# Performance work log

Hardware: AMD Instinct MI355X
Metric: run time of the kernel (lower is better)

Reference implementation:

```python
import jax, jax.numpy as jnp
import numpy as np

FP8_MAX = 448.0   # e4m3 max finite value
BLOCK = 128


def _cast_e4m3(v):
    """Fake-cast to fp8 e4m3: round to nearest representable value (3 mantissa bits,
    min normal exponent -6, subnormal step 2^-9), saturate at +-448."""
    a = jnp.minimum(jnp.abs(v), FP8_MAX)
    e = jnp.floor(jnp.log2(jnp.maximum(a, jnp.float32(2.0) ** -9)))
    e = jnp.maximum(e, -6.0)                 # subnormal range
    step = jnp.exp2(e - 3.0)                 # 3 mantissa bits
    q = jnp.round(a / step) * step
    q = jnp.minimum(q, FP8_MAX)
    return jnp.sign(v) * q


def fake_quant_blockwise(x, br, bc):
    """Per-(br x bc)-tile scale = amax/448, cast to e4m3, dequantize."""
    R, C = x.shape
    xt = x.reshape(R // br, br, C // bc, bc)
    amax = jnp.max(jnp.abs(xt), axis=(1, 3), keepdims=True)
    scale = jnp.maximum(amax, 1e-12) / FP8_MAX
    q = _cast_e4m3(xt / scale) * scale
    return q.reshape(R, C)


def setup_inputs() -> dict:
    key = jax.random.key(0)
    k1, k2 = jax.random.split(key)
    x = jax.random.normal(k1, (8192, 4096), dtype=jnp.float32)
    weight = jax.random.normal(k2, (4096, 4096), dtype=jnp.float32) * 0.02
    bias = jnp.zeros((4096,), dtype=jnp.float32)
    return {"x": x, "weight": weight, "bias": bias}


def reference(x, weight, bias):
    # activations: per-row 1x128 blocks (is_left); weight: 128x128 square tiles (is_sqtile)
    x_fq = fake_quant_blockwise(x, 1, BLOCK)
    w_fq = fake_quant_blockwise(weight, BLOCK, BLOCK)
    return jnp.einsum('ti,oi->to', x_fq, w_fq) + bias
```

## Files before the change

### kernel.cpp

```cpp
#include <hip/hip_runtime.h>

#define M_DIM 8192
#define N_DIM 4096
#define K_DIM 4096

typedef __bf16 bf16x8 __attribute__((ext_vector_type(8)));
typedef float f32x4 __attribute__((ext_vector_type(4)));

__device__ __forceinline__ unsigned short f2bf(float f) {
    unsigned u = __float_as_uint(f);
    u += 0x7FFFu + ((u >> 16) & 1u);
    return (unsigned short)(u >> 16);
}

__device__ __forceinline__ float cast_e4m3(float v) {
    float a = fminf(fabsf(v), 448.0f);
    float am = fmaxf(a, 0x1p-9f);
    int e = (int)((__float_as_uint(am) >> 23) & 0xFFu) - 127;
    e = (e < -6) ? -6 : e;
    float step = __uint_as_float((unsigned)(e - 3 + 127) << 23);
    float q = rintf(a / step) * step;
    q = fminf(q, 448.0f);
    return (v < 0.0f) ? -q : q;
}

__global__ __launch_bounds__(256) void quant_x(const float* __restrict__ X,
                                               unsigned short* __restrict__ Xq) {
    const int g = threadIdx.x >> 5;
    const int l = threadIdx.x & 31;
    const long rb = (long)blockIdx.x * 8 + g;
    const int row = (int)(rb >> 5);
    const int kb = (int)(rb & 31);
    const size_t base = (size_t)row * K_DIM + kb * 128 + l * 4;
    const float4 v = *(const float4*)&X[base];
    float amax = fmaxf(fmaxf(fabsf(v.x), fabsf(v.y)), fmaxf(fabsf(v.z), fabsf(v.w)));
    #pragma unroll
    for (int m = 16; m >= 1; m >>= 1)
        amax = fmaxf(amax, __shfl_xor(amax, m));
    const float scale = fmaxf(amax, 1e-12f) / 448.0f;
    ushort4 o;
    o.x = f2bf(cast_e4m3(v.x / scale) * scale);
    o.y = f2bf(cast_e4m3(v.y / scale) * scale);
    o.z = f2bf(cast_e4m3(v.z / scale) * scale);
    o.w = f2bf(cast_e4m3(v.w / scale) * scale);
    *(ushort4*)&Xq[base] = o;
}

__global__ __launch_bounds__(256) void quant_w(const float* __restrict__ W,
                                               unsigned short* __restrict__ Wq) {
    const int tile = blockIdx.x;
    const int tr = tile >> 5;
    const int tc = tile & 31;
    const int t = threadIdx.x;
    const int c4 = (t & 31) * 4;
    const float* base = W + (size_t)(tr * 128) * K_DIM + tc * 128;

    float4 v[16];
    float amax = 0.0f;
    #pragma unroll
    for (int p = 0; p < 16; ++p) {
        const int r = p * 8 + (t >> 5);
        v[p] = *(const float4*)&base[(size_t)r * K_DIM + c4];
        amax = fmaxf(amax, fmaxf(fmaxf(fabsf(v[p].x), fabsf(v[p].y)),
                                 fmaxf(fabsf(v[p].z), fabsf(v[p].w))));
    }
    #pragma unroll
    for (int m = 32; m >= 1; m >>= 1)
        amax = fmaxf(amax, __shfl_xor(amax, m));
    __shared__ float red[4];
    if ((t & 63) == 0) red[t >> 6] = amax;
    __syncthreads();
    const float am4 = fmaxf(fmaxf(red[0], red[1]), fmaxf(red[2], red[3]));
    const float scale = fmaxf(am4, 1e-12f) / 448.0f;

    unsigned short* out = Wq + (size_t)(tr * 128) * K_DIM + tc * 128;
    #pragma unroll
    for (int p = 0; p < 16; ++p) {
        const int r = p * 8 + (t >> 5);
        ushort4 o;
        o.x = f2bf(cast_e4m3(v[p].x / scale) * scale);
        o.y = f2bf(cast_e4m3(v[p].y / scale) * scale);
        o.z = f2bf(cast_e4m3(v[p].z / scale) * scale);
        o.w = f2bf(cast_e4m3(v[p].w / scale) * scale);
        *(ushort4*)&out[(size_t)r * K_DIM + c4] = o;
    }
}

#define GLOAD16(g, l)                                                          \
    __builtin_amdgcn_global_load_lds(                                          \
        (const __attribute__((address_space(1))) void*)(g),                    \
        (__attribute__((address_space(3))) void*)(l), 16, 0, 0)


#define BARRIER() __builtin_amdgcn_s_barrier()
#define LGKM0() asm volatile("s_waitcnt lgkmcnt(0)" ::: "memory")
#define LGKM8() asm volatile("s_waitcnt lgkmcnt(8)" ::: "memory")
#define VM6()   asm volatile("s_waitcnt vmcnt(6)" ::: "memory")
#define VM0()   asm volatile("s_waitcnt vmcnt(0)" ::: "memory")

#define STAGE(G, grow0, kt, ebase, ht) do {                                    \
    const int _kt = (kt) > 63 ? 63 : (kt);                                     \
    const unsigned short* _s0 = (G) +                                          \
        (size_t)((grow0) + (ht) * 128 + w * 8 + sr) * K_DIM + _kt * 64 + src_col; \
    const unsigned short* _s1 = _s0 + (size_t)64 * K_DIM;                      \
    char* _lb = (char*)lds + (ebase) * 2 + ((ht) * 128 + w * 8) * 128;         \
    GLOAD16(_s0, _lb);                                                         \
    GLOAD16(_s1, _lb + 8192);                                                  \
} while (0)

#define LDA(mh, ebase) do {                                                    \
    _Pragma("unroll") for (int _m = 0; _m < 4; ++_m) {                         \
        const int _row = wm * 128 + (mh) * 64 + _m * 16 + lr;                  \
        a[_m][0] = *(const bf16x8*)&lds[(ebase) + _row * 64 + ((0  + hk) ^ rsw)]; \
        a[_m][1] = *(const bf16x8*)&lds[(ebase) + _row * 64 + ((32 + hk) ^ rsw)]; \
    }                                                                          \
} while (0)

#define LDB(nh, dst, ebase) do {                                               \
    _Pragma("unroll") for (int _n = 0; _n < 2; ++_n) {                         \
        const int _row = wn * 64 + (nh) * 32 + _n * 16 + lr;                   \
        dst[_n][0] = *(const bf16x8*)&lds[(ebase) + _row * 64 + ((0  + hk) ^ rsw)]; \
        dst[_n][1] = *(const bf16x8*)&lds[(ebase) + _row * 64 + ((32 + hk) ^ rsw)]; \
    }                                                                          \
} while (0)

#define MMA(mh, nh, bb) do {                                                   \
    _Pragma("unroll") for (int _m = 0; _m < 4; ++_m)                           \
    _Pragma("unroll") for (int _n = 0; _n < 2; ++_n)                           \
    _Pragma("unroll") for (int _k = 0; _k < 2; ++_k)                           \
        acc[(mh) * 4 + _m][(nh) * 2 + _n] =                                    \
            __builtin_amdgcn_mfma_f32_16x16x32_bf16(                           \
                a[_m][_k], bb[_n][_k], acc[(mh) * 4 + _m][(nh) * 2 + _n], 0, 0, 0); \
} while (0)

#define PRIO1() __builtin_amdgcn_s_setprio(1)
#define PRIO0() __builtin_amdgcn_s_setprio(0)

__global__ __launch_bounds__(512, 2) void gemm256(const unsigned short* __restrict__ A,
                                                  const unsigned short* __restrict__ B,
                                                  const float* __restrict__ bias,
                                                  float* __restrict__ C) {
    __shared__ __align__(16) unsigned short lds[65536];

    const int t = threadIdx.x;
    const int lane = t & 63;
    const int w = t >> 6;
    const int wm = w >> 2, wn = w & 3;

    int bid = blockIdx.x;
    bid = (bid & 7) * 64 + (bid >> 3);
    const int bm = bid >> 4, bn = bid & 15;
    const size_t brow = (size_t)bm * 256, bcol = (size_t)bn * 256;

    const int sr = lane >> 3;
    const int src_col = (((lane & 7) ^ ((lane >> 3) & 7)) << 3);
    const int lr = lane & 15;
    const int hk = (lane >> 4) * 8;
    const int rsw = (lane & 7) << 3;

    f32x4 acc[8][4] = {};
    bf16x8 a[4][2], b0[2][2], b1[2][2];

    STAGE(A, brow, 0, 0, 0);     STAGE(A, brow, 0, 0, 1);
    STAGE(B, bcol, 0, 32768, 0); STAGE(B, bcol, 0, 32768, 1);
    STAGE(B, bcol, 1, 49152, 0); STAGE(B, bcol, 1, 49152, 1);
    STAGE(A, brow, 1, 16384, 0);
    VM6(); BARRIER();

    for (int u = 0; u < 64; u += 2) {
        LDA(0, 0); LDB(0, b0, 32768); LDB(1, b1, 32768);
        STAGE(A, brow, u + 1, 16384, 1);
        LGKM8();
        BARRIER(); LGKM0();
        PRIO1(); MMA(0, 0, b0); PRIO0();
        BARRIER();
        STAGE(B, bcol, u + 2, 32768, 0);
        BARRIER();
        PRIO1(); MMA(0, 1, b1); PRIO0();
        BARRIER();
        LDA(1, 0);
        STAGE(B, bcol, u + 2, 32768, 1);
        BARRIER(); LGKM0();
        PRIO1(); MMA(1, 1, b1); PRIO0();
        BARRIER();
        STAGE(A, brow, u + 2, 0, 0);
        BARRIER();
        PRIO1(); MMA(1, 0, b0); PRIO0();
        VM6();
        BARRIER();
        LDA(0, 16384); LDB(0, b0, 49152); LDB(1, b1, 49152);
        STAGE(A, brow, u + 2, 0, 1);
        LGKM8();
        BARRIER(); LGKM0();
        PRIO1(); MMA(0, 0, b0); PRIO0();
        BARRIER();
        STAGE(B, bcol, u + 3, 49152, 0);
        BARRIER();
        PRIO1(); MMA(0, 1, b1); PRIO0();
        BARRIER();
        LDA(1, 16384);
        STAGE(B, bcol, u + 3, 49152, 1);
        BARRIER(); LGKM0();
        PRIO1(); MMA(1, 1, b1); PRIO0();
        BARRIER();
        STAGE(A, brow, u + 3, 16384, 0);
        BARRIER();
        PRIO1(); MMA(1, 0, b0); PRIO0();
        VM6();
        BARRIER();
    }

    VM0();

    #pragma unroll
    for (int i = 0; i < 8; ++i) {
        const size_t row_base = brow + wm * 128 + i * 16 + (lane >> 4) * 4;
        #pragma unroll
        for (int j = 0; j < 4; ++j) {
            const size_t col = bcol + wn * 64 + j * 16 + lr;
            const float bv = bias[col];
            #pragma unroll
            for (int jj = 0; jj < 4; ++jj)
                C[(row_base + jj) * (size_t)N_DIM + col] = acc[i][j][jj] + bv;
        }
    }
}

extern "C" void kernel_launch(void* const* d_in, const int* in_sizes, int n_in,
                              void* d_out, int out_size, void* d_ws, size_t ws_size,
                              hipStream_t stream) {
    const float* x = (const float*)d_in[0];
    const float* w = (const float*)d_in[1];
    const float* bias = (const float*)d_in[2];
    float* out = (float*)d_out;

    unsigned short* xq = (unsigned short*)d_ws;
    unsigned short* wq = xq + (size_t)M_DIM * K_DIM;

    quant_x<<<(M_DIM * (K_DIM / 128)) / 8, 256, 0, stream>>>(x, xq);
    quant_w<<<(N_DIM / 128) * (K_DIM / 128), 256, 0, stream>>>(w, wq);
    gemm256<<<(M_DIM / 256) * (N_DIM / 256), 512, 0, stream>>>(xq, wq, bias, out);
}
```

Measured before the change: 293.8 us.

## Double-buffer LDS fragment registers to overlap reads with MFMA in GEMM loop

Rewrites the GEMM main loop schedule to use separate register fragments (a0/a1, b0e/b0o) so LDS reads for the next sub-tile are issued before the current MFMA block. It also cuts the barriers per half-iteration from eight to four and replaces full lgkmcnt(0) waits with partial counts. The point is to hide LDS latency and barrier stalls behind matrix instructions. The cost is more live registers, and the finer wait counts may hide ordering hazards between async global-to-LDS loads and reads.

```diff
diff --git a/kernel.cpp b/kernel.cpp
--- a/kernel.cpp
+++ b/kernel.cpp
@@ -93,10 +93,11 @@
 
 
 #define BARRIER() __builtin_amdgcn_s_barrier()
-#define LGKM0() asm volatile("s_waitcnt lgkmcnt(0)" ::: "memory")
-#define LGKM8() asm volatile("s_waitcnt lgkmcnt(8)" ::: "memory")
-#define VM6()   asm volatile("s_waitcnt vmcnt(6)" ::: "memory")
-#define VM0()   asm volatile("s_waitcnt vmcnt(0)" ::: "memory")
+#define FENCE()  asm volatile("" ::: "memory")
+#define LGKM(n)  asm volatile("s_waitcnt lgkmcnt(" #n ")" ::: "memory")
+#define VMC(n)   asm volatile("s_waitcnt vmcnt(" #n ")" ::: "memory")
+#define PRIO1()  __builtin_amdgcn_s_setprio(1)
+#define PRIO0()  __builtin_amdgcn_s_setprio(0)
 
 #define STAGE(G, grow0, kt, ebase, ht) do {                                    \
     const int _kt = (kt) > 63 ? 63 : (kt);                                     \
@@ -108,15 +109,15 @@
     GLOAD16(_s1, _lb + 8192);                                                  \
 } while (0)
 
-#define LDA(mh, ebase) do {                                                    \
+#define LDA(dst, mh, ebase) do {                                               \
     _Pragma("unroll") for (int _m = 0; _m < 4; ++_m) {                         \
         const int _row = wm * 128 + (mh) * 64 + _m * 16 + lr;                  \
-        a[_m][0] = *(const bf16x8*)&lds[(ebase) + _row * 64 + ((0  + hk) ^ rsw)]; \
-        a[_m][1] = *(const bf16x8*)&lds[(ebase) + _row * 64 + ((32 + hk) ^ rsw)]; \
+        dst[_m][0] = *(const bf16x8*)&lds[(ebase) + _row * 64 + ((0  + hk) ^ rsw)]; \
+        dst[_m][1] = *(const bf16x8*)&lds[(ebase) + _row * 64 + ((32 + hk) ^ rsw)]; \
     }                                                                          \
 } while (0)
 
-#define LDB(nh, dst, ebase) do {                                               \
+#define LDB(dst, nh, ebase) do {                                               \
     _Pragma("unroll") for (int _n = 0; _n < 2; ++_n) {                         \
         const int _row = wn * 64 + (nh) * 32 + _n * 16 + lr;                   \
         dst[_n][0] = *(const bf16x8*)&lds[(ebase) + _row * 64 + ((0  + hk) ^ rsw)]; \
@@ -124,17 +125,19 @@
     }                                                                          \
 } while (0)
 
-#define MMA(mh, nh, bb) do {                                                   \
+#define MMA(aA, mh, nh, bB) do {                                               \
     _Pragma("unroll") for (int _m = 0; _m < 4; ++_m)                           \
     _Pragma("unroll") for (int _n = 0; _n < 2; ++_n)                           \
     _Pragma("unroll") for (int _k = 0; _k < 2; ++_k)                           \
         acc[(mh) * 4 + _m][(nh) * 2 + _n] =                                    \
             __builtin_amdgcn_mfma_f32_16x16x32_bf16(                           \
-                a[_m][_k], bb[_n][_k], acc[(mh) * 4 + _m][(nh) * 2 + _n], 0, 0, 0); \
-} while (0)
-
-#define PRIO1() __builtin_amdgcn_s_setprio(1)
-#define PRIO0() __builtin_amdgcn_s_setprio(0)
+                aA[_m][_k], bB[_n][_k], acc[(mh) * 4 + _m][(nh) * 2 + _n], 0, 0, 0); \
+} while (0)
+
+#define AE 0
+#define AO 16384
+#define BE 32768
+#define BO 49152
 
 __global__ __launch_bounds__(512, 2) void gemm256(const unsigned short* __restrict__ A,
                                                   const unsigned short* __restrict__ B,
@@ -159,58 +162,57 @@
     const int rsw = (lane & 7) << 3;
 
     f32x4 acc[8][4] = {};
-    bf16x8 a[4][2], b0[2][2], b1[2][2];
-
-    STAGE(A, brow, 0, 0, 0);     STAGE(A, brow, 0, 0, 1);
-    STAGE(B, bcol, 0, 32768, 0); STAGE(B, bcol, 0, 32768, 1);
-    STAGE(B, bcol, 1, 49152, 0); STAGE(B, bcol, 1, 49152, 1);
-    STAGE(A, brow, 1, 16384, 0);
-    VM6(); BARRIER();
+    bf16x8 a0[4][2], a1[4][2], b0e[2][2], b0o[2][2], b1[2][2];
+
+    STAGE(A, brow, 0, AE, 0); STAGE(A, brow, 0, AE, 1);
+    STAGE(B, bcol, 0, BE, 0); STAGE(B, bcol, 0, BE, 1);
+    STAGE(B, bcol, 1, BO, 0); STAGE(B, bcol, 1, BO, 1);
+    VMC(4); BARRIER(); FENCE();
+    LDA(a0, 0, AE); LDB(b0e, 0, BE);
+    FENCE();
 
     for (int u = 0; u < 64; u += 2) {
-        LDA(0, 0); LDB(0, b0, 32768); LDB(1, b1, 32768);
-        STAGE(A, brow, u + 1, 16384, 1);
-        LGKM8();
-        BARRIER(); LGKM0();
-        PRIO1(); MMA(0, 0, b0); PRIO0();
-        BARRIER();
-        STAGE(B, bcol, u + 2, 32768, 0);
-        BARRIER();
-        PRIO1(); MMA(0, 1, b1); PRIO0();
-        BARRIER();
-        LDA(1, 0);
-        STAGE(B, bcol, u + 2, 32768, 1);
-        BARRIER(); LGKM0();
-        PRIO1(); MMA(1, 1, b1); PRIO0();
-        BARRIER();
-        STAGE(A, brow, u + 2, 0, 0);
-        BARRIER();
-        PRIO1(); MMA(1, 0, b0); PRIO0();
-        VM6();
-        BARRIER();
-        LDA(0, 16384); LDB(0, b0, 49152); LDB(1, b1, 49152);
-        STAGE(A, brow, u + 2, 0, 1);
-        LGKM8();
-        BARRIER(); LGKM0();
-        PRIO1(); MMA(0, 0, b0); PRIO0();
-        BARRIER();
-        STAGE(B, bcol, u + 3, 49152, 0);
-        BARRIER();
-        PRIO1(); MMA(0, 1, b1); PRIO0();
-        BARRIER();
-        LDA(1, 16384);
-        STAGE(B, bcol, u + 3, 49152, 1);
-        BARRIER(); LGKM0();
-        PRIO1(); MMA(1, 1, b1); PRIO0();
-        BARRIER();
-        STAGE(A, brow, u + 3, 16384, 0);
-        BARRIER();
-        PRIO1(); MMA(1, 0, b0); PRIO0();
-        VM6();
-        BARRIER();
-    }
-
-    VM0();
+        LDB(b1, 1, BE);
+        STAGE(A, brow, u + 1, AO, 0); STAGE(A, brow, u + 1, AO, 1);
+        LGKM(4);
+        PRIO1(); MMA(a0, 0, 0, b0e); PRIO0();
+        BARRIER(); FENCE();
+        LDA(a1, 1, AE);
+        LGKM(8);
+        PRIO1(); MMA(a0, 0, 1, b1); PRIO0();
+        BARRIER(); FENCE();
+        STAGE(B, bcol, u + 2, BE, 0);
+        LGKM(0);
+        PRIO1(); MMA(a1, 1, 1, b1); PRIO0();
+        VMC(2);
+        BARRIER(); FENCE();
+        LDA(a0, 0, AO); LDB(b0o, 0, BO);
+        STAGE(B, bcol, u + 2, BE, 1);
+        PRIO1(); MMA(a1, 1, 0, b0e); PRIO0();
+        BARRIER(); FENCE();
+
+        LDB(b1, 1, BO);
+        STAGE(A, brow, u + 2, AE, 0); STAGE(A, brow, u + 2, AE, 1);
+        LGKM(4);
+        PRIO1(); MMA(a0, 0, 0, b0o); PRIO0();
+        BARRIER(); FENCE();
+        LDA(a1, 1, AO);
+        LGKM(8);
+        PRIO1(); MMA(a0, 0, 1, b1); PRIO0();
+        BARRIER(); FENCE();
+        STAGE(B, bcol, u + 3, BO, 0);
+        LGKM(0);
+        PRIO1(); MMA(a1, 1, 1, b1); PRIO0();
+        VMC(2);
+        BARRIER(); FENCE();
+        LDA(a0, 0, AE); LDB(b0e, 0, BE);
+        STAGE(B, bcol, u + 3, BO, 1);
+        PRIO1(); MMA(a1, 1, 0, b0o); PRIO0();
+        BARRIER(); FENCE();
+    }
+
+    LGKM(0); VMC(0);
+    BARRIER();
 
     #pragma unroll
     for (int i = 0; i < 8; ++i) {
```

Measured after the change: 324.9 us. +10.6%, slower.

## Halve GEMM K-tile to 32 and shrink LDS to 64KB

Applied to the files above, without the earlier changes.

Changes the main bf16 GEMM's K step from 64 to 32, so each stage holds half the data and LDS drops from 128KB to 64KB. The load swizzle, wait counts and stage schedule are reworked to match, and the loop runs twice as many iterations. The smaller LDS footprint may ease occupancy or scheduling with two blocks per CU. In exchange there are twice as many barriers and loop iterations per unit of MMA work, and less latency hiding per stage.

```diff
diff --git a/kernel.cpp b/kernel.cpp
--- a/kernel.cpp
+++ b/kernel.cpp
@@ -94,53 +94,50 @@
 
 #define BARRIER() __builtin_amdgcn_s_barrier()
 #define LGKM0() asm volatile("s_waitcnt lgkmcnt(0)" ::: "memory")
-#define LGKM8() asm volatile("s_waitcnt lgkmcnt(8)" ::: "memory")
-#define VM6()   asm volatile("s_waitcnt vmcnt(6)" ::: "memory")
+#define VM2()   asm volatile("s_waitcnt vmcnt(2)" ::: "memory")
 #define VM0()   asm volatile("s_waitcnt vmcnt(0)" ::: "memory")
+#define PRIO1() __builtin_amdgcn_s_setprio(1)
+#define PRIO0() __builtin_amdgcn_s_setprio(0)
 
 #define STAGE(G, grow0, kt, ebase, ht) do {                                    \
-    const int _kt = (kt) > 63 ? 63 : (kt);                                     \
-    const unsigned short* _s0 = (G) +                                          \
-        (size_t)((grow0) + (ht) * 128 + w * 8 + sr) * K_DIM + _kt * 64 + src_col; \
-    const unsigned short* _s1 = _s0 + (size_t)64 * K_DIM;                      \
-    char* _lb = (char*)lds + (ebase) * 2 + ((ht) * 128 + w * 8) * 128;         \
-    GLOAD16(_s0, _lb);                                                         \
-    GLOAD16(_s1, _lb + 8192);                                                  \
+    const int _kt = (kt) > 127 ? 127 : (kt);                                   \
+    const unsigned short* _s = (G) +                                           \
+        (size_t)((grow0) + (ht) * 128 + (t >> 2)) * K_DIM + _kt * 32 + src_e;  \
+    GLOAD16(_s, (char*)lds + (ebase) * 2 + (ht) * 8192 + w * 1024);            \
 } while (0)
 
 #define LDA(mh, ebase) do {                                                    \
     _Pragma("unroll") for (int _m = 0; _m < 4; ++_m) {                         \
         const int _row = wm * 128 + (mh) * 64 + _m * 16 + lr;                  \
-        a[_m][0] = *(const bf16x8*)&lds[(ebase) + _row * 64 + ((0  + hk) ^ rsw)]; \
-        a[_m][1] = *(const bf16x8*)&lds[(ebase) + _row * 64 + ((32 + hk) ^ rsw)]; \
+        a[_m] = *(const bf16x8*)&lds[(ebase) + _row * 32 + rde];               \
     }                                                                          \
 } while (0)
 
 #define LDB(nh, dst, ebase) do {                                               \
     _Pragma("unroll") for (int _n = 0; _n < 2; ++_n) {                         \
         const int _row = wn * 64 + (nh) * 32 + _n * 16 + lr;                   \
-        dst[_n][0] = *(const bf16x8*)&lds[(ebase) + _row * 64 + ((0  + hk) ^ rsw)]; \
-        dst[_n][1] = *(const bf16x8*)&lds[(ebase) + _row * 64 + ((32 + hk) ^ rsw)]; \
+        dst[_n] = *(const bf16x8*)&lds[(ebase) + _row * 32 + rde];             \
     }                                                                          \
 } while (0)
 
 #define MMA(mh, nh, bb) do {                                                   \
     _Pragma("unroll") for (int _m = 0; _m < 4; ++_m)                           \
     _Pragma("unroll") for (int _n = 0; _n < 2; ++_n)                           \
-    _Pragma("unroll") for (int _k = 0; _k < 2; ++_k)                           \
         acc[(mh) * 4 + _m][(nh) * 2 + _n] =                                    \
             __builtin_amdgcn_mfma_f32_16x16x32_bf16(                           \
-                a[_m][_k], bb[_n][_k], acc[(mh) * 4 + _m][(nh) * 2 + _n], 0, 0, 0); \
-} while (0)
-
-#define PRIO1() __builtin_amdgcn_s_setprio(1)
-#define PRIO0() __builtin_amdgcn_s_setprio(0)
+                a[_m], bb[_n], acc[(mh) * 4 + _m][(nh) * 2 + _n], 0, 0, 0);    \
+} while (0)
+
+#define A0E 0
+#define A1E 8192
+#define B0E 16384
+#define B1E 24576
 
 __global__ __launch_bounds__(512, 2) void gemm256(const unsigned short* __restrict__ A,
                                                   const unsigned short* __restrict__ B,
                                                   const float* __restrict__ bias,
                                                   float* __restrict__ C) {
-    __shared__ __align__(16) unsigned short lds[65536];
+    __shared__ __align__(16) unsigned short lds[32768];
 
     const int t = threadIdx.x;
     const int lane = t & 63;
@@ -152,61 +149,58 @@
     const int bm = bid >> 4, bn = bid & 15;
     const size_t brow = (size_t)bm * 256, bcol = (size_t)bn * 256;
 
-    const int sr = lane >> 3;
-    const int src_col = (((lane & 7) ^ ((lane >> 3) & 7)) << 3);
+    const int src_e = ((lane & 3) ^ ((t >> 3) & 3)) * 8;
     const int lr = lane & 15;
-    const int hk = (lane >> 4) * 8;
-    const int rsw = (lane & 7) << 3;
+    const int rde = (((lane >> 4) ^ (lane >> 1)) & 3) << 3;
 
     f32x4 acc[8][4] = {};
-    bf16x8 a[4][2], b0[2][2], b1[2][2];
-
-    STAGE(A, brow, 0, 0, 0);     STAGE(A, brow, 0, 0, 1);
-    STAGE(B, bcol, 0, 32768, 0); STAGE(B, bcol, 0, 32768, 1);
-    STAGE(B, bcol, 1, 49152, 0); STAGE(B, bcol, 1, 49152, 1);
-    STAGE(A, brow, 1, 16384, 0);
-    VM6(); BARRIER();
-
-    for (int u = 0; u < 64; u += 2) {
-        LDA(0, 0); LDB(0, b0, 32768); LDB(1, b1, 32768);
-        STAGE(A, brow, u + 1, 16384, 1);
-        LGKM8();
+    bf16x8 a[4], b0[2], b1[2];
+
+    STAGE(A, brow, 0, A0E, 0); STAGE(A, brow, 0, A0E, 1);
+    STAGE(B, bcol, 0, B0E, 0); STAGE(B, bcol, 0, B0E, 1);
+    STAGE(B, bcol, 1, B1E, 0); STAGE(B, bcol, 1, B1E, 1);
+    VM2(); BARRIER();
+
+    for (int u = 0; u < 128; u += 2) {
+        LDA(0, A0E); LDB(0, b0, B0E);
+        STAGE(A, brow, u + 1, A1E, 0);
         BARRIER(); LGKM0();
         PRIO1(); MMA(0, 0, b0); PRIO0();
         BARRIER();
-        STAGE(B, bcol, u + 2, 32768, 0);
-        BARRIER();
+        LDB(1, b1, B0E);
+        STAGE(A, brow, u + 1, A1E, 1);
+        BARRIER(); LGKM0();
         PRIO1(); MMA(0, 1, b1); PRIO0();
         BARRIER();
-        LDA(1, 0);
-        STAGE(B, bcol, u + 2, 32768, 1);
+        LDA(1, A0E);
+        STAGE(B, bcol, u + 2, B0E, 0);
         BARRIER(); LGKM0();
         PRIO1(); MMA(1, 1, b1); PRIO0();
         BARRIER();
-        STAGE(A, brow, u + 2, 0, 0);
+        STAGE(B, bcol, u + 2, B0E, 1);
         BARRIER();
         PRIO1(); MMA(1, 0, b0); PRIO0();
-        VM6();
-        BARRIER();
-        LDA(0, 16384); LDB(0, b0, 49152); LDB(1, b1, 49152);
-        STAGE(A, brow, u + 2, 0, 1);
-        LGKM8();
+        VM2();
+        BARRIER();
+        LDA(0, A1E); LDB(0, b0, B1E);
+        STAGE(A, brow, u + 2, A0E, 0);
         BARRIER(); LGKM0();
         PRIO1(); MMA(0, 0, b0); PRIO0();
         BARRIER();
-        STAGE(B, bcol, u + 3, 49152, 0);
-        BARRIER();
+        LDB(1, b1, B1E);
+        STAGE(A, brow, u + 2, A0E, 1);
+        BARRIER(); LGKM0();
         PRIO1(); MMA(0, 1, b1); PRIO0();
         BARRIER();
-        LDA(1, 16384);
-        STAGE(B, bcol, u + 3, 49152, 1);
+        LDA(1, A1E);
+        STAGE(B, bcol, u + 3, B1E, 0);
         BARRIER(); LGKM0();
         PRIO1(); MMA(1, 1, b1); PRIO0();
         BARRIER();
-        STAGE(A, brow, u + 3, 16384, 0);
+        STAGE(B, bcol, u + 3, B1E, 1);
         BARRIER();
         PRIO1(); MMA(1, 0, b0); PRIO0();
-        VM6();
+        VM2();
         BARRIER();
     }
 
```

Result: slower. 304.3 us (+3.6%).

## Switch GEMM inner loop to 32x32x16 bf16 MFMA with rescheduled staging

Applied to the files above, without the earlier changes.

Replaces the 16x16x32 MFMA tiles with 32x32x16 MFMA instructions, changing the per-wave fragment layout, LDS read pattern, and epilogue store mapping. The prefetch schedule is also reordered so LDS reads are interleaved between MFMA groups, with a different vmcnt wait depth. The larger MFMA shape is meant to cut the number of LDS fragment reads and instructions per FLOP. In exchange it changes the staging order and the output store pattern, which may affect latency hiding and write coalescing.

```diff
diff --git a/kernel.cpp b/kernel.cpp
--- a/kernel.cpp
+++ b/kernel.cpp
@@ -5,7 +5,7 @@
 #define K_DIM 4096
 
 typedef __bf16 bf16x8 __attribute__((ext_vector_type(8)));
-typedef float f32x4 __attribute__((ext_vector_type(4)));
+typedef float f32x16 __attribute__((ext_vector_type(16)));
 
 __device__ __forceinline__ unsigned short f2bf(float f) {
     unsigned u = __float_as_uint(f);
@@ -95,8 +95,10 @@
 #define BARRIER() __builtin_amdgcn_s_barrier()
 #define LGKM0() asm volatile("s_waitcnt lgkmcnt(0)" ::: "memory")
 #define LGKM8() asm volatile("s_waitcnt lgkmcnt(8)" ::: "memory")
-#define VM6()   asm volatile("s_waitcnt vmcnt(6)" ::: "memory")
+#define VM4()   asm volatile("s_waitcnt vmcnt(4)" ::: "memory")
 #define VM0()   asm volatile("s_waitcnt vmcnt(0)" ::: "memory")
+#define PRIO1() __builtin_amdgcn_s_setprio(1)
+#define PRIO0() __builtin_amdgcn_s_setprio(0)
 
 #define STAGE(G, grow0, kt, ebase, ht) do {                                    \
     const int _kt = (kt) > 63 ? 63 : (kt);                                     \
@@ -108,33 +110,28 @@
     GLOAD16(_s1, _lb + 8192);                                                  \
 } while (0)
 
-#define LDA(mh, ebase) do {                                                    \
-    _Pragma("unroll") for (int _m = 0; _m < 4; ++_m) {                         \
-        const int _row = wm * 128 + (mh) * 64 + _m * 16 + lr;                  \
-        a[_m][0] = *(const bf16x8*)&lds[(ebase) + _row * 64 + ((0  + hk) ^ rsw)]; \
-        a[_m][1] = *(const bf16x8*)&lds[(ebase) + _row * 64 + ((32 + hk) ^ rsw)]; \
+#define LDA32(mh) do {                                                         \
+    _Pragma("unroll") for (int _f = 0; _f < 2; ++_f) {                         \
+        const int _row = wm * 128 + (mh) * 64 + _f * 32 + l31;                 \
+        _Pragma("unroll") for (int _k = 0; _k < 4; ++_k)                       \
+            a[_f][_k] = *(const bf16x8*)&lds[abase + _row * 64 +               \
+                                             ((_k * 16 + hk32) ^ rsw)];        \
     }                                                                          \
 } while (0)
 
-#define LDB(nh, dst, ebase) do {                                               \
-    _Pragma("unroll") for (int _n = 0; _n < 2; ++_n) {                         \
-        const int _row = wn * 64 + (nh) * 32 + _n * 16 + lr;                   \
-        dst[_n][0] = *(const bf16x8*)&lds[(ebase) + _row * 64 + ((0  + hk) ^ rsw)]; \
-        dst[_n][1] = *(const bf16x8*)&lds[(ebase) + _row * 64 + ((32 + hk) ^ rsw)]; \
-    }                                                                          \
-} while (0)
-
-#define MMA(mh, nh, bb) do {                                                   \
-    _Pragma("unroll") for (int _m = 0; _m < 4; ++_m)                           \
-    _Pragma("unroll") for (int _n = 0; _n < 2; ++_n)                           \
-    _Pragma("unroll") for (int _k = 0; _k < 2; ++_k)                           \
-        acc[(mh) * 4 + _m][(nh) * 2 + _n] =                                    \
-            __builtin_amdgcn_mfma_f32_16x16x32_bf16(                           \
-                a[_m][_k], bb[_n][_k], acc[(mh) * 4 + _m][(nh) * 2 + _n], 0, 0, 0); \
-} while (0)
-
-#define PRIO1() __builtin_amdgcn_s_setprio(1)
-#define PRIO0() __builtin_amdgcn_s_setprio(0)
+#define LDB32(nh, dst) do {                                                    \
+    const int _row = wn * 64 + (nh) * 32 + l31;                                \
+    _Pragma("unroll") for (int _k = 0; _k < 4; ++_k)                           \
+        dst[_k] = *(const bf16x8*)&lds[bbase + _row * 64 +                     \
+                                       ((_k * 16 + hk32) ^ rsw)];              \
+} while (0)
+
+#define MMA32(mh, nh, bb) do {                                                 \
+    _Pragma("unroll") for (int _k = 0; _k < 4; ++_k)                           \
+    _Pragma("unroll") for (int _f = 0; _f < 2; ++_f)                           \
+        acc[(mh) * 2 + _f][nh] = __builtin_amdgcn_mfma_f32_32x32x16_bf16(      \
+            a[_f][_k], bb[_k], acc[(mh) * 2 + _f][nh], 0, 0, 0);               \
+} while (0)
 
 __global__ __launch_bounds__(512, 2) void gemm256(const unsigned short* __restrict__ A,
                                                   const unsigned short* __restrict__ B,
@@ -154,74 +151,81 @@
 
     const int sr = lane >> 3;
     const int src_col = (((lane & 7) ^ ((lane >> 3) & 7)) << 3);
-    const int lr = lane & 15;
-    const int hk = (lane >> 4) * 8;
+    const int l31 = lane & 31;
+    const int hk32 = (lane >> 5) * 8;
     const int rsw = (lane & 7) << 3;
 
-    f32x4 acc[8][4] = {};
-    bf16x8 a[4][2], b0[2][2], b1[2][2];
+    f32x16 acc[4][2] = {};
+    bf16x8 a[2][4], b0[4], b1[4];
+    int abase, bbase;
 
     STAGE(A, brow, 0, 0, 0);     STAGE(A, brow, 0, 0, 1);
     STAGE(B, bcol, 0, 32768, 0); STAGE(B, bcol, 0, 32768, 1);
     STAGE(B, bcol, 1, 49152, 0); STAGE(B, bcol, 1, 49152, 1);
-    STAGE(A, brow, 1, 16384, 0);
-    VM6(); BARRIER();
+    VM4(); BARRIER();
 
     for (int u = 0; u < 64; u += 2) {
-        LDA(0, 0); LDB(0, b0, 32768); LDB(1, b1, 32768);
+        abase = 0; bbase = 32768;
+        LDA32(0); LDB32(0, b0);
+        STAGE(A, brow, u + 1, 16384, 0);
+        LGKM8();
+        BARRIER(); LGKM0();
+        PRIO1(); MMA32(0, 0, b0); PRIO0();
+        BARRIER();
+        LDB32(1, b1);
         STAGE(A, brow, u + 1, 16384, 1);
+        BARRIER(); LGKM0();
+        PRIO1(); MMA32(0, 1, b1); PRIO0();
+        BARRIER();
+        LDA32(1);
+        STAGE(B, bcol, u + 2, 32768, 0);
+        BARRIER(); LGKM0();
+        PRIO1(); MMA32(1, 1, b1); PRIO0();
+        BARRIER();
+        STAGE(B, bcol, u + 2, 32768, 1);
+        BARRIER();
+        PRIO1(); MMA32(1, 0, b0); PRIO0();
+        VM4();
+        BARRIER();
+        abase = 16384; bbase = 49152;
+        LDA32(0); LDB32(0, b0);
+        STAGE(A, brow, u + 2, 0, 0);
         LGKM8();
         BARRIER(); LGKM0();
-        PRIO1(); MMA(0, 0, b0); PRIO0();
-        BARRIER();
-        STAGE(B, bcol, u + 2, 32768, 0);
-        BARRIER();
-        PRIO1(); MMA(0, 1, b1); PRIO0();
-        BARRIER();
-        LDA(1, 0);
-        STAGE(B, bcol, u + 2, 32768, 1);
-        BARRIER(); LGKM0();
-        PRIO1(); MMA(1, 1, b1); PRIO0();
-        BARRIER();
-        STAGE(A, brow, u + 2, 0, 0);
-        BARRIER();
-        PRIO1(); MMA(1, 0, b0); PRIO0();
-        VM6();
-        BARRIER();
-        LDA(0, 16384); LDB(0, b0, 49152); LDB(1, b1, 49152);
+        PRIO1(); MMA32(0, 0, b0); PRIO0();
+        BARRIER();
+        LDB32(1, b1);
         STAGE(A, brow, u + 2, 0, 1);
-        LGKM8();
-        BARRIER(); LGKM0();
-        PRIO1(); MMA(0, 0, b0); PRIO0();
-        BARRIER();
+        BARRIER(); LGKM0();
+        PRIO1(); MMA32(0, 1, b1); PRIO0();
+        BARRIER();
+        LDA32(1);
         STAGE(B, bcol, u + 3, 49152, 0);
-        BARRIER();
-        PRIO1(); MMA(0, 1, b1); PRIO0();
-        BARRIER();
-        LDA(1, 16384);
+        BARRIER(); LGKM0();
+        PRIO1(); MMA32(1, 1, b1); PRIO0();
+        BARRIER();
         STAGE(B, bcol, u + 3, 49152, 1);
-        BARRIER(); LGKM0();
-        PRIO1(); MMA(1, 1, b1); PRIO0();
-        BARRIER();
-        STAGE(A, brow, u + 3, 16384, 0);
-        BARRIER();
-        PRIO1(); MMA(1, 0, b0); PRIO0();
-        VM6();
+        BARRIER();
+        PRIO1(); MMA32(1, 0, b0); PRIO0();
+        VM4();
         BARRIER();
     }
 
     VM0();
 
-    #pragma unroll
-    for (int i = 0; i < 8; ++i) {
-        const size_t row_base = brow + wm * 128 + i * 16 + (lane >> 4) * 4;
+    const int hi4 = (lane >> 5) * 4;
+    #pragma unroll
+    for (int fr = 0; fr < 4; ++fr) {
         #pragma unroll
-        for (int j = 0; j < 4; ++j) {
-            const size_t col = bcol + wn * 64 + j * 16 + lr;
+        for (int fc = 0; fc < 2; ++fc) {
+            const size_t col = bcol + wn * 64 + fc * 32 + l31;
             const float bv = bias[col];
             #pragma unroll
-            for (int jj = 0; jj < 4; ++jj)
-                C[(row_base + jj) * (size_t)N_DIM + col] = acc[i][j][jj] + bv;
+            for (int reg = 0; reg < 16; ++reg) {
+                const size_t row = brow + wm * 128 + fr * 32 +
+                                   (reg & 3) + 8 * (reg >> 2) + hi4;
+                C[row * (size_t)N_DIM + col] = acc[fr][fc][reg] + bv;
+            }
         }
     }
 }
```

New measurement: 328.4 us. +11.8%, slower.
